# Performance work log

Measured on AMD Instinct MI355X. Metric: run time of the kernel, lower is better.

The kernel has to match this reference:

```python
import jax, jax.numpy as jnp
import numpy as np

H = 256    # hidden_size
NH = 8     # num_heads
B = 256    # batch_size (num graphs)
M = 128    # max_num_nodes per graph
N = B * M  # total nodes
E = N * 16 # total edges


def _bn(x, g, b, eps=1e-5):
    # BatchNorm1d in training mode: batch stats over node dim, biased variance
    m = x.mean(0)
    v = ((x - m) ** 2).mean(0)
    return g * (x - m) * jax.lax.rsqrt(v + eps) + b


def setup_inputs() -> dict:
    key = jax.random.key(0)
    ks = jax.random.split(key, 12)
    def lin(k, o, i):
        return jax.random.normal(k, (o, i), jnp.float32) / np.sqrt(i).astype(np.float32)
    return {
        "h": jax.random.normal(ks[0], (N, H), jnp.float32),
        "gin_w1": lin(ks[1], H, H), "gin_b1": jnp.zeros((H,), jnp.float32),
        "gin_w2": lin(ks[2], H, H), "gin_b2": jnp.zeros((H,), jnp.float32),
        "in_proj_w": lin(ks[3], 3 * H, H), "in_proj_b": jnp.zeros((3 * H,), jnp.float32),
        "out_proj_w": lin(ks[4], H, H), "out_proj_b": jnp.zeros((H,), jnp.float32),
        "bn_local_g": jnp.ones((H,), jnp.float32), "bn_local_b": jnp.zeros((H,), jnp.float32),
        "bn_attn_g": jnp.ones((H,), jnp.float32), "bn_attn_b": jnp.zeros((H,), jnp.float32),
        "bn_out_g": jnp.ones((H,), jnp.float32), "bn_out_b": jnp.zeros((H,), jnp.float32),
        "ffn1_w": lin(ks[5], 2 * H, H), "ffn1_b": jnp.zeros((2 * H,), jnp.float32),
        "ffn2_w": lin(ks[6], H, 2 * H), "ffn2_b": jnp.zeros((H,), jnp.float32),
        "edge_src": jax.random.randint(ks[7], (E,), 0, N, dtype=jnp.int32),
        "edge_dst": jax.random.randint(ks[8], (E,), 0, N, dtype=jnp.int32),
        "batch_num_nodes": jnp.full((B,), M, dtype=jnp.int32),
    }


def reference(h, gin_w1, gin_b1, gin_w2, gin_b2, in_proj_w, in_proj_b,
              out_proj_w, out_proj_b, bn_local_g, bn_local_b, bn_attn_g, bn_attn_b,
              bn_out_g, bn_out_b, ffn1_w, ffn1_b, ffn2_w, ffn2_b,
              edge_src, edge_dst, batch_num_nodes):
    # ---- local GIN conv: gin_nn((1+eps)*h + sum_neighbors h), eps=0 ----
    agg = jax.ops.segment_sum(h[edge_src], edge_dst, num_segments=N)
    z = h + agg
    z = jax.nn.relu(z @ gin_w1.T + gin_b1) @ gin_w2.T + gin_b2
    h_local = _bn(h + z, bn_local_g, bn_local_b)  # dropout=0

    # ---- to_dense_batch scatter indices ----
    cum = jnp.concatenate([jnp.zeros((1,), batch_num_nodes.dtype), jnp.cumsum(batch_num_nodes)])
    node = jnp.arange(N, dtype=jnp.int32)
    bid = jnp.searchsorted(cum[1:], node, side='right')  # graph id per node
    idx = node - cum[bid] + bid * M                      # slot in dense [B*M]
    hd = jnp.zeros((B * M, H), h.dtype).at[idx].set(h).reshape(B, M, H)
    mask = jnp.zeros((B * M,), bool).at[idx].set(True).reshape(B, M)

    # ---- MultiheadAttention (batch_first, self-attn, key_padding_mask) ----
    qkv = hd @ in_proj_w.T + in_proj_b
    q, k, v = jnp.split(qkv, 3, axis=-1)
    dh = H // NH
    q = q.reshape(B, M, NH, dh)
    k = k.reshape(B, M, NH, dh)
    v = v.reshape(B, M, NH, dh)
    scores = jnp.einsum('bqhd,bkhd->bhqk', q, k) / np.float32(np.sqrt(dh))
    scores = jnp.where(mask[:, None, None, :], scores, jnp.float32(-1e9))
    attn = jax.nn.softmax(scores, axis=-1)
    ao = jnp.einsum('bhqk,bkhd->bqhd', attn, v).reshape(B, M, H)
    ao = ao @ out_proj_w.T + out_proj_b
    h_attn = ao.reshape(B * M, H)[idx]  # ragged gather back (x[mask])
    h_attn = _bn(h + h_attn, bn_attn_g, bn_attn_b)

    # ---- combine + FFN + out norm ----
    hh = h_local + h_attn
    hh = hh + (jax.nn.relu(hh @ ffn1_w.T + ffn1_b) @ ffn2_w.T + ffn2_b)
    return _bn(hh, bn_out_g, bn_out_b)
```

## Files before the change

kernel.cpp:

```cpp
#include <hip/hip_runtime.h>

#define NNODES 32768
#define HDIM   256
#define NHEADS 8
#define NB     256
#define NEDGES 524288


typedef unsigned short u16;
typedef unsigned int   u32;
typedef unsigned long long u64;
typedef __attribute__((ext_vector_type(8))) short short8;
typedef __attribute__((ext_vector_type(4))) float f32x4;

__device__ __forceinline__ float bf2f(u16 u){
  union { u32 i; float f; } x; x.i = ((u32)u) << 16; return x.f;
}
__device__ __forceinline__ u16 f2bf(float f){
  union { float f; u32 i; } x; x.f = f;
  u32 r = x.i + 0x7fffu + ((x.i >> 16) & 1u);
  return (u16)(r >> 16);
}
__device__ __forceinline__ void unpack8(uint4 v, float* f){
  f[0] = bf2f((u16)(v.x & 0xffff)); f[1] = bf2f((u16)(v.x >> 16));
  f[2] = bf2f((u16)(v.y & 0xffff)); f[3] = bf2f((u16)(v.y >> 16));
  f[4] = bf2f((u16)(v.z & 0xffff)); f[5] = bf2f((u16)(v.z >> 16));
  f[6] = bf2f((u16)(v.w & 0xffff)); f[7] = bf2f((u16)(v.w >> 16));
}
__device__ __forceinline__ uint4 pack8(const float* f){
  uint4 v;
  v.x = (u32)f2bf(f[0]) | ((u32)f2bf(f[1]) << 16);
  v.y = (u32)f2bf(f[2]) | ((u32)f2bf(f[3]) << 16);
  v.z = (u32)f2bf(f[4]) | ((u32)f2bf(f[5]) << 16);
  v.w = (u32)f2bf(f[6]) | ((u32)f2bf(f[7]) << 16);
  return v;
}

typedef __attribute__((address_space(3))) unsigned int lds_u32;
typedef const __attribute__((address_space(1))) unsigned int gbl_u32;
__device__ __forceinline__ void gload16(const void* g, void* l){
  __builtin_amdgcn_global_load_lds((gbl_u32*)(u64)g,
                                   (lds_u32*)(u32)(u64)l, 16, 0, 0);
}

struct CvtPtrs { const void* p[19]; };

__device__ static const int CVT_CH[19] = {
  2097152,16384,64,16384,64,49152,192,16384,64,64,64,64,64,64,64,32768,128,32768,64};
__device__ static const int CVT_PR[19] = {
  0,8388608,8454144,8454400,8519936,8520192,8716800,8717568,8783104,
  8783360,8783616,8783872,8784128,8784384,8784640,8784896,8915968,8916480,9047552};
#define CVT_TOTAL_CHUNKS 2261952

__global__ __launch_bounds__(256) void convert_k(CvtPtrs cp, u16* __restrict__ dst,
    const int* __restrict__ edge_dst, int* __restrict__ counts){
  int gid = blockIdx.x * 256 + threadIdx.x;
  if (gid < NEDGES) atomicAdd(&counts[edge_dst[gid]], 1);
  if (gid >= CVT_TOTAL_CHUNKS) return;
  int t = 0, rem = gid;
  while (t < 18 && rem >= CVT_CH[t]) { rem -= CVT_CH[t]; t++; }
  u16* d = dst + CVT_PR[t] + (size_t)rem * 4;
  float4 v = ((const float4*)cp.p[t])[rem];
  u16 o[4] = { f2bf(v.x), f2bf(v.y), f2bf(v.z), f2bf(v.w) };
  *(uint2*)d = *(const uint2*)o;
}

__global__ void scan_k(const int* __restrict__ counts, int* __restrict__ offsets,
                       int* __restrict__ cursor){
  __shared__ int part[1024];
  int t = threadIdx.x;
  int local[32];
  int s = 0;
  int base = t * 32;
#pragma unroll
  for (int i = 0; i < 32; i++){ local[i] = counts[base + i]; s += local[i]; }
  part[t] = s;
  __syncthreads();
  for (int off = 1; off < 1024; off <<= 1){
    int v = (t >= off) ? part[t - off] : 0;
    __syncthreads();
    part[t] += v;
    __syncthreads();
  }
  int run = part[t] - s;
#pragma unroll
  for (int i = 0; i < 32; i++){
    offsets[base + i] = run; cursor[base + i] = run; run += local[i];
  }
  if (t == 1023) offsets[NNODES] = run;
}

__global__ void bucket_k(const int* __restrict__ src, const int* __restrict__ dst,
                         int* __restrict__ cursor, int* __restrict__ srcs){
  int e = blockIdx.x * 256 + threadIdx.x;
  int p = atomicAdd(&cursor[dst[e]], 1);
  srcs[p] = src[e];
}

__global__ __launch_bounds__(256) void agg_k(const u16* __restrict__ h,
    const int* __restrict__ offsets, const int* __restrict__ srcs,
    u16* __restrict__ z0){
  int node = blockIdx.x * 4 + (threadIdx.x >> 6);
  int lane = threadIdx.x & 63;
  size_t coff = (size_t)lane * 4;
  int beg = offsets[node], end = offsets[node + 1];

  uint2 self = *(const uint2*)&h[(size_t)node * HDIM + coff];
  float a0 = bf2f((u16)(self.x & 0xffff)), a1 = bf2f((u16)(self.x >> 16));
  float a2 = bf2f((u16)(self.y & 0xffff)), a3 = bf2f((u16)(self.y >> 16));

  int e = beg;
  for (; e + 8 <= end; e += 8){
    uint2 v[8];
#pragma unroll
    for (int i = 0; i < 8; i++){
      int s = srcs[e + i];
      v[i] = *(const uint2*)&h[(size_t)s * HDIM + coff];
    }
#pragma unroll
    for (int i = 0; i < 8; i++){
      a0 += bf2f((u16)(v[i].x & 0xffff));
      a1 += bf2f((u16)(v[i].x >> 16));
      a2 += bf2f((u16)(v[i].y & 0xffff));
      a3 += bf2f((u16)(v[i].y >> 16));
    }
  }
  for (; e < end; e++){
    int s = srcs[e];
    uint2 va = *(const uint2*)&h[(size_t)s * HDIM + coff];
    a0 += bf2f((u16)(va.x & 0xffff));
    a1 += bf2f((u16)(va.x >> 16));
    a2 += bf2f((u16)(va.y & 0xffff));
    a3 += bf2f((u16)(va.y >> 16));
  }

  uint2 o;
  o.x = (u32)f2bf(a0) | ((u32)f2bf(a1) << 16);
  o.y = (u32)f2bf(a2) | ((u32)f2bf(a3) << 16);
  *(uint2*)&z0[(size_t)node * HDIM + coff] = o;
}

__device__ __forceinline__ void mfma_step(const u16* AS_, const u16* WS_,
    f32x4 (&acc)[4][4], int wm, int wn, int ln, int q4){
  short8 af[4], bfr[4];
#pragma unroll
  for (int mt = 0; mt < 4; mt++)
    af[mt] = *(const short8*)&AS_[(wm * 64 + mt * 16 + ln) * 32 + q4 * 8];
#pragma unroll
  for (int nt = 0; nt < 4; nt++)
    bfr[nt] = *(const short8*)&WS_[(wn * 64 + nt * 16 + ln) * 32 + q4 * 8];
#pragma unroll
  for (int mt = 0; mt < 4; mt++)
#pragma unroll
    for (int nt = 0; nt < 4; nt++)
      acc[mt][nt] = __builtin_amdgcn_mfma_f32_16x16x32_bf16(af[mt], bfr[nt], acc[mt][nt], 0, 0, 0);
}

template<int NO, int K, bool RELU, bool RES, bool STATS>
__global__ __launch_bounds__(256) void gemm_bt(const u16* __restrict__ A,
    const u16* __restrict__ W, const u16* __restrict__ bias,
    const u16* __restrict__ res, u16* __restrict__ C,
    float* __restrict__ ssum, float* __restrict__ ssq){
  __shared__ u16 As0[4096], Ws0[4096], As1[4096], Ws1[4096];
  const int tid = threadIdx.x;
  const int m0 = blockIdx.y * 128;
  const int n0 = blockIdx.x * 128;
  const int wave = tid >> 6, lane = tid & 63;
  const int wm = wave >> 1, wn = wave & 1;
  const int q4 = lane >> 4, ln = lane & 15;

  f32x4 acc[4][4] = {};

  const int r_l = tid >> 2;
  const int c_l = (tid & 3) * 8;
  const u16* gA = A + (size_t)(m0 + r_l) * K + c_l;
  const u16* gW = W + (size_t)(n0 + r_l) * K + c_l;
  u16* dA0 = As0 + wave * 512; u16* dW0 = Ws0 + wave * 512;
  u16* dA1 = As1 + wave * 512; u16* dW1 = Ws1 + wave * 512;

  const int NT = K / 32;

  gload16(gA, dA0); gload16(gA + 64 * K, dA0 + 2048);
  gload16(gW, dW0); gload16(gW + 64 * K, dW0 + 2048);
  __syncthreads();

#pragma unroll
  for (int t = 0; t < NT; t += 2){
    if (t + 1 < NT){
      int kn = (t + 1) * 32;
      gload16(gA + kn, dA1); gload16(gA + 64 * K + kn, dA1 + 2048);
      gload16(gW + kn, dW1); gload16(gW + 64 * K + kn, dW1 + 2048);
    }
    mfma_step(As0, Ws0, acc, wm, wn, ln, q4);
    __syncthreads();
    if (t + 2 < NT){
      int kn = (t + 2) * 32;
      gload16(gA + kn, dA0); gload16(gA + 64 * K + kn, dA0 + 2048);
      gload16(gW + kn, dW0); gload16(gW + 64 * K + kn, dW0 + 2048);
    }
    mfma_step(As1, Ws1, acc, wm, wn, ln, q4);
    __syncthreads();
  }

#pragma unroll
  for (int nt = 0; nt < 4; nt++){
    int col = n0 + wn * 64 + nt * 16 + ln;
    float bv = bf2f(bias[col]);
    float cs = 0.0f, cq = 0.0f;
#pragma unroll
    for (int mt = 0; mt < 4; mt++){
      int row = m0 + wm * 64 + mt * 16 + q4 * 4;
#pragma unroll
      for (int reg = 0; reg < 4; reg++){
        float v = acc[mt][nt][reg] + bv;
        if (RELU) v = fmaxf(v, 0.0f);
        if (RES)  v += bf2f(res[(size_t)(row + reg) * NO + col]);
        C[(size_t)(row + reg) * NO + col] = f2bf(v);
        if (STATS){ cs += v; cq += v * v; }
      }
    }
    if (STATS){
      cs += __shfl_xor(cs, 16); cs += __shfl_xor(cs, 32);
      cq += __shfl_xor(cq, 16); cq += __shfl_xor(cq, 32);
      if (lane < 16){
        atomicAdd(&ssum[col], cs);
        atomicAdd(&ssq[col], cq);
      }
    }
  }
}

__global__ __launch_bounds__(256) void attn_k(const u16* __restrict__ qkv,
                                              u16* __restrict__ ao){
  __shared__ u16 Qs[128 * 40];
  __shared__ u16 Ks[128 * 40];
  __shared__ u16 VTs[32 * 136];
  __shared__ u16 Ps[128 * 136];

  const int b  = blockIdx.x >> 3;
  const int nh = blockIdx.x & 7;
  const int tid = threadIdx.x;
  const int wave = tid >> 6, lane = tid & 63;
  const int q4 = lane >> 4, ln = lane & 15;

#pragma unroll
  for (int c2 = 0; c2 < 2; c2++){
    int chunk = tid + c2 * 256;
    int r = chunk >> 2;
    int cc = chunk & 3;
    size_t nb = (size_t)(b * 128 + r) * 768 + nh * 32 + cc * 8;
    uint4 vq = *(const uint4*)&qkv[nb];
    uint4 vk = *(const uint4*)&qkv[nb + 256];
    uint4 vv = *(const uint4*)&qkv[nb + 512];
    *(uint4*)&Qs[r * 40 + cc * 8] = vq;
    *(uint4*)&Ks[r * 40 + cc * 8] = vk;
    union { uint4 v; u16 h[8]; } uv; uv.v = vv;
#pragma unroll
    for (int i = 0; i < 8; i++) VTs[(cc * 8 + i) * 136 + r] = uv.h[i];
  }
  __syncthreads();

  f32x4 accs[2][8] = {};
  short8 qf[2];
#pragma unroll
  for (int mt = 0; mt < 2; mt++)
    qf[mt] = *(const short8*)&Qs[(wave * 32 + mt * 16 + ln) * 40 + q4 * 8];
#pragma unroll
  for (int nt = 0; nt < 8; nt++){
    short8 kf = *(const short8*)&Ks[(nt * 16 + ln) * 40 + q4 * 8];
    accs[0][nt] = __builtin_amdgcn_mfma_f32_16x16x32_bf16(qf[0], kf, accs[0][nt], 0, 0, 0);
    accs[1][nt] = __builtin_amdgcn_mfma_f32_16x16x32_bf16(qf[1], kf, accs[1][nt], 0, 0, 0);
  }

  const float scale = 0.17677669529663687f;
  float invs[2][4];
#pragma unroll
  for (int mt = 0; mt < 2; mt++){
#pragma unroll
    for (int reg = 0; reg < 4; reg++){
      float rm = -1e30f;
#pragma unroll
      for (int nt = 0; nt < 8; nt++){
        accs[mt][nt][reg] *= scale;
        rm = fmaxf(rm, accs[mt][nt][reg]);
      }
      for (int m = 1; m < 16; m <<= 1) rm = fmaxf(rm, __shfl_xor(rm, m));
      float rs = 0.0f;
#pragma unroll
      for (int nt = 0; nt < 8; nt++){
        float e = __expf(accs[mt][nt][reg] - rm);
        accs[mt][nt][reg] = e;
        rs += e;
      }
      for (int m = 1; m < 16; m <<= 1) rs += __shfl_xor(rs, m);
      invs[mt][reg] = 1.0f / rs;
    }
  }

#pragma unroll
  for (int mt = 0; mt < 2; mt++)
#pragma unroll
    for (int nt = 0; nt < 8; nt++)
#pragma unroll
      for (int reg = 0; reg < 4; reg++)
        Ps[(wave * 32 + mt * 16 + q4 * 4 + reg) * 136 + nt * 16 + ln] =
            f2bf(accs[mt][nt][reg] * invs[mt][reg]);
  __syncthreads();

  f32x4 acco[2][2] = {};
#pragma unroll
  for (int kk = 0; kk < 4; kk++){
    short8 pf[2], vf[2];
#pragma unroll
    for (int mt = 0; mt < 2; mt++)
      pf[mt] = *(const short8*)&Ps[(wave * 32 + mt * 16 + ln) * 136 + kk * 32 + q4 * 8];
#pragma unroll
    for (int nt = 0; nt < 2; nt++)
      vf[nt] = *(const short8*)&VTs[(nt * 16 + ln) * 136 + kk * 32 + q4 * 8];
#pragma unroll
    for (int mt = 0; mt < 2; mt++)
#pragma unroll
      for (int nt = 0; nt < 2; nt++)
        acco[mt][nt] = __builtin_amdgcn_mfma_f32_16x16x32_bf16(pf[mt], vf[nt], acco[mt][nt], 0, 0, 0);
  }

#pragma unroll
  for (int mt = 0; mt < 2; mt++)
#pragma unroll
    for (int nt = 0; nt < 2; nt++)
#pragma unroll
      for (int reg = 0; reg < 4; reg++){
        int node = b * 128 + wave * 32 + mt * 16 + q4 * 4 + reg;
        int col = nh * 32 + nt * 16 + ln;
        ao[(size_t)node * HDIM + col] = f2bf(acco[mt][nt][reg]);
      }
}

__global__ __launch_bounds__(256) void combine_k(const u16* __restrict__ xl,
    const u16* __restrict__ xa, const float* __restrict__ stats,
    const u16* __restrict__ gl, const u16* __restrict__ bl,
    const u16* __restrict__ ga, const u16* __restrict__ ba,
    u16* __restrict__ hh){
  __shared__ float cs0[256], cs1[256], cs2[256];
  int t = threadIdx.x;
  {
    const float invN = 1.0f / 32768.0f;
    float mA = stats[t] * invN;
    float vA = stats[256 + t] * invN - mA * mA;
    float sA = bf2f(gl[t]) * rsqrtf(vA + 1e-5f);
    float tA = bf2f(bl[t]) - mA * sA;
    float mB = stats[512 + t] * invN;
    float vB = stats[768 + t] * invN - mB * mB;
    float sB = bf2f(ga[t]) * rsqrtf(vB + 1e-5f);
    float tB = bf2f(ba[t]) - mB * sB;
    cs0[t] = sA; cs1[t] = sB; cs2[t] = tA + tB;
  }
  __syncthreads();
  int gid = blockIdx.x * 256 + t;
  size_t off = (size_t)gid * 8;
  int cb = (int)(off & 255);
  float sl[8], sa[8], tt[8];
  *(float4*)&sl[0] = *(const float4*)&cs0[cb];
  *(float4*)&sl[4] = *(const float4*)&cs0[cb + 4];
  *(float4*)&sa[0] = *(const float4*)&cs1[cb];
  *(float4*)&sa[4] = *(const float4*)&cs1[cb + 4];
  *(float4*)&tt[0] = *(const float4*)&cs2[cb];
  *(float4*)&tt[4] = *(const float4*)&cs2[cb + 4];
  float fl[8], fa[8], fo[8];
  unpack8(*(const uint4*)&xl[off], fl);
  unpack8(*(const uint4*)&xa[off], fa);
#pragma unroll
  for (int i = 0; i < 8; i++) fo[i] = sl[i] * fl[i] + sa[i] * fa[i] + tt[i];
  *(uint4*)&hh[off] = pack8(fo);
}

__global__ __launch_bounds__(256) void finalbn_k(const u16* __restrict__ y,
    const float* __restrict__ stats, const u16* __restrict__ g,
    const u16* __restrict__ bb, float* __restrict__ out){
  __shared__ float cs0[256], cs1[256];
  int t = threadIdx.x;
  {
    const float invN = 1.0f / 32768.0f;
    float m = stats[1024 + t] * invN;
    float v = stats[1280 + t] * invN - m * m;
    float s = bf2f(g[t]) * rsqrtf(v + 1e-5f);
    cs0[t] = s; cs1[t] = bf2f(bb[t]) - m * s;
  }
  __syncthreads();
  int gid = blockIdx.x * 256 + t;
  size_t off = (size_t)gid * 8;
  int cb = (int)(off & 255);
  float ss[8], tt[8];
  *(float4*)&ss[0] = *(const float4*)&cs0[cb];
  *(float4*)&ss[4] = *(const float4*)&cs0[cb + 4];
  *(float4*)&tt[0] = *(const float4*)&cs1[cb];
  *(float4*)&tt[4] = *(const float4*)&cs1[cb + 4];
  float fy[8], fo[8];
  unpack8(*(const uint4*)&y[off], fy);
#pragma unroll
  for (int i = 0; i < 8; i++) fo[i] = ss[i] * fy[i] + tt[i];
  *(float4*)&out[off] = *(const float4*)&fo[0];
  *(float4*)&out[off + 4] = *(const float4*)&fo[4];
}

extern "C" void kernel_launch(void* const* d_in, const int* in_sizes, int n_in,
                              void* d_out, int out_size, void* d_ws, size_t ws_size,
                              hipStream_t stream){
  const int* edge_src = (const int*)d_in[19];
  const int* edge_dst = (const int*)d_in[20];

  char* ws = (char*)d_ws;
  float* stats = (float*)ws;
  u16*   conv  = (u16*)(ws + 12288);
  u16*   A     = (u16*)(ws + 12288 + 18095616);
  u16*   B     = (u16*)(ws + 12288 + 18095616 + 16777216);
  u16*   C     = (u16*)d_out;
  const size_t BIG_NEED = 51662336ull + 50331648ull;
  const bool big = (ws_size >= BIG_NEED);
  u16* QKV = (u16*)(ws + 51662336);

  int* counts  = (int*)B;
  int* offsets = (int*)((char*)B + 131072);
  int* cursor  = (int*)((char*)B + 262400);
  int* srcs    = (int*)((char*)B + 393472);

  const u16* convH = conv;
  const u16* W1  = conv + 8388608; const u16* b1g = conv + 8454144;
  const u16* W2  = conv + 8454400; const u16* b2g = conv + 8519936;
  const u16* Win = conv + 8520192; const u16* bin = conv + 8716800;
  const u16* Wo  = conv + 8717568; const u16* bo  = conv + 8783104;
  const u16* g_l = conv + 8783360; const u16* b_l = conv + 8783616;
  const u16* g_a = conv + 8783872; const u16* b_a = conv + 8784128;
  const u16* g_o = conv + 8784384; const u16* b_o = conv + 8784640;
  const u16* Wf1 = conv + 8784896; const u16* bf1 = conv + 8915968;
  const u16* Wf2 = conv + 8916480; const u16* bf2 = conv + 9047552;

  hipMemsetAsync(ws, 0, 6144, stream);
  hipMemsetAsync(counts, 0, 131072, stream);

  CvtPtrs cp;
  for (int i = 0; i < 19; i++) cp.p[i] = d_in[i];
  convert_k<<<8836, 256, 0, stream>>>(cp, conv, edge_dst, counts);

  scan_k<<<1, 1024, 0, stream>>>(counts, offsets, cursor);
  bucket_k<<<NEDGES / 256, 256, 0, stream>>>(edge_src, edge_dst, cursor, srcs);
  agg_k<<<NNODES / 4, 256, 0, stream>>>(convH, offsets, srcs, A);

  gemm_bt<256, 256, true,  false, false><<<dim3(2, 256), 256, 0, stream>>>(
      A, W1, b1g, nullptr, B, nullptr, nullptr);
  gemm_bt<256, 256, false, true,  true ><<<dim3(2, 256), 256, 0, stream>>>(
      B, W2, b2g, convH, A, stats + 0, stats + 256);

  if (big){
    gemm_bt<768, 256, false, false, false><<<dim3(6, 256), 256, 0, stream>>>(
        convH, Win, bin, nullptr, QKV, nullptr, nullptr);
    attn_k<<<2048, 256, 0, stream>>>(QKV, C);
  } else {
    for (int c = 0; c < 4; c++){
      const u16* hA = convH + (size_t)c * 8192 * HDIM;
      u16* aoC = C + (size_t)c * 8192 * HDIM;
      gemm_bt<768, 256, false, false, false><<<dim3(6, 64), 256, 0, stream>>>(
          hA, Win, bin, nullptr, B, nullptr, nullptr);
      attn_k<<<512, 256, 0, stream>>>(B, aoC);
    }
  }

  gemm_bt<256, 256, false, true, true><<<dim3(2, 256), 256, 0, stream>>>(
      C, Wo, bo, convH, B, stats + 512, stats + 768);

  combine_k<<<4096, 256, 0, stream>>>(A, B, stats, g_l, b_l, g_a, b_a, C);

  gemm_bt<512, 256, true,  false, false><<<dim3(4, 256), 256, 0, stream>>>(
      C, Wf1, bf1, nullptr, A, nullptr, nullptr);
  gemm_bt<256, 512, false, true,  true ><<<dim3(2, 256), 256, 0, stream>>>(
      A, Wf2, bf2, C, (u16*)conv, stats + 1024, stats + 1280);

  finalbn_k<<<4096, 256, 0, stream>>>(conv, stats, g_o, b_o, (float*)d_out);
}
```

Baseline: 424.6 us.

## Stage GEMM and attention epilogues through LDS, fuse GIN1 with QKV GEMM

GEMM epilogues now write results into swizzled shared memory and then emit coalesced 16-byte global stores, with residual tiles also loaded into LDS in coalesced form. The attention output goes through LDS the same way. In the big-workspace path, the first GIN GEMM and the QKV projection share one launch (gemm_dual), and the stats memset is folded into scan_k. The aim is to replace scattered 2-byte stores and loads with coalesced vector traffic and to cut launches, at the cost of extra LDS traffic and barriers. The relu flag becomes a runtime value instead of a template parameter.

```diff
diff --git a/kernel.cpp b/kernel.cpp
--- a/kernel.cpp
+++ b/kernel.cpp
@@ -66,9 +66,11 @@
 }
 
 __global__ void scan_k(const int* __restrict__ counts, int* __restrict__ offsets,
-                       int* __restrict__ cursor){
+                       int* __restrict__ cursor, float* __restrict__ stats){
   __shared__ int part[1024];
   int t = threadIdx.x;
+  stats[t] = 0.0f;
+  if (t < 512) stats[1024 + t] = 0.0f;
   int local[32];
   int s = 0;
   int base = t * 32;
@@ -156,28 +158,21 @@
       acc[mt][nt] = __builtin_amdgcn_mfma_f32_16x16x32_bf16(af[mt], bfr[nt], acc[mt][nt], 0, 0, 0);
 }
 
-template<int NO, int K, bool RELU, bool RES, bool STATS>
-__global__ __launch_bounds__(256) void gemm_bt(const u16* __restrict__ A,
-    const u16* __restrict__ W, const u16* __restrict__ bias,
-    const u16* __restrict__ res, u16* __restrict__ C,
-    float* __restrict__ ssum, float* __restrict__ ssq){
-  __shared__ u16 As0[4096], Ws0[4096], As1[4096], Ws1[4096];
-  const int tid = threadIdx.x;
-  const int m0 = blockIdx.y * 128;
-  const int n0 = blockIdx.x * 128;
+template<int K>
+__device__ __forceinline__ void kloop(const u16* __restrict__ A,
+    const u16* __restrict__ W, u16* smem, int m0, int n0, int tid,
+    f32x4 (&acc)[4][4]){
+  u16* As0 = smem;        u16* Ws0 = smem + 4096;
+  u16* As1 = smem + 8192; u16* Ws1 = smem + 12288;
   const int wave = tid >> 6, lane = tid & 63;
   const int wm = wave >> 1, wn = wave & 1;
   const int q4 = lane >> 4, ln = lane & 15;
-
-  f32x4 acc[4][4] = {};
-
   const int r_l = tid >> 2;
   const int c_l = (tid & 3) * 8;
   const u16* gA = A + (size_t)(m0 + r_l) * K + c_l;
   const u16* gW = W + (size_t)(n0 + r_l) * K + c_l;
   u16* dA0 = As0 + wave * 512; u16* dW0 = Ws0 + wave * 512;
   u16* dA1 = As1 + wave * 512; u16* dW1 = Ws1 + wave * 512;
-
   const int NT = K / 32;
 
   gload16(gA, dA0); gload16(gA + 64 * K, dA0 + 2048);
@@ -201,21 +196,51 @@
     mfma_step(As1, Ws1, acc, wm, wn, ln, q4);
     __syncthreads();
   }
+}
+
+struct GemmCfg {
+  const u16* A; const u16* W; const u16* bias; const u16* res;
+  u16* C; float* ssum; float* ssq;
+  int NO; int nx; int relu;
+};
+
+template<bool RES, bool STATS>
+__device__ __forceinline__ void epilogue(f32x4 (&acc)[4][4], u16* smem,
+    const GemmCfg& c, int m0, int n0, int tid){
+  const int NO = c.NO;
+  const int wave = tid >> 6, lane = tid & 63;
+  const int wm = wave >> 1, wn = wave & 1;
+  const int q4 = lane >> 4, ln = lane & 15;
+
+  if (RES){
+#pragma unroll
+    for (int i = 0; i < 8; i++){
+      int ch = tid + i * 256;
+      int r = ch >> 4, k = ch & 15;
+      uint4 vv = *(const uint4*)&c.res[(size_t)(m0 + r) * NO + n0 + (k << 3)];
+      *(uint4*)&smem[r * 128 + ((((k >> 1) ^ (r & 7)) << 4)) + ((k & 1) << 3)] = vv;
+    }
+    __syncthreads();
+  }
 
 #pragma unroll
   for (int nt = 0; nt < 4; nt++){
-    int col = n0 + wn * 64 + nt * 16 + ln;
-    float bv = bf2f(bias[col]);
+    int lcol = wn * 64 + nt * 16 + ln;
+    int gcol = n0 + lcol;
+    float bv = bf2f(c.bias[gcol]);
+    int chunk = lcol >> 4;
     float cs = 0.0f, cq = 0.0f;
 #pragma unroll
     for (int mt = 0; mt < 4; mt++){
-      int row = m0 + wm * 64 + mt * 16 + q4 * 4;
+      int lrow = wm * 64 + mt * 16 + q4 * 4;
 #pragma unroll
       for (int reg = 0; reg < 4; reg++){
+        int r = lrow + reg;
+        int sidx = r * 128 + ((chunk ^ (r & 7)) << 4) + ln;
         float v = acc[mt][nt][reg] + bv;
-        if (RELU) v = fmaxf(v, 0.0f);
-        if (RES)  v += bf2f(res[(size_t)(row + reg) * NO + col]);
-        C[(size_t)(row + reg) * NO + col] = f2bf(v);
+        if (c.relu) v = fmaxf(v, 0.0f);
+        if (RES) v += bf2f(smem[sidx]);
+        smem[sidx] = f2bf(v);
         if (STATS){ cs += v; cq += v * v; }
       }
     }
@@ -223,11 +248,44 @@
       cs += __shfl_xor(cs, 16); cs += __shfl_xor(cs, 32);
       cq += __shfl_xor(cq, 16); cq += __shfl_xor(cq, 32);
       if (lane < 16){
-        atomicAdd(&ssum[col], cs);
-        atomicAdd(&ssq[col], cq);
+        atomicAdd(&c.ssum[gcol], cs);
+        atomicAdd(&c.ssq[gcol], cq);
       }
     }
   }
+  __syncthreads();
+
+#pragma unroll
+  for (int i = 0; i < 8; i++){
+    int ch = tid + i * 256;
+    int r = ch >> 4, k = ch & 15;
+    uint4 vv = *(const uint4*)&smem[r * 128 + (((k >> 1) ^ (r & 7)) << 4) + ((k & 1) << 3)];
+    *(uint4*)&c.C[(size_t)(m0 + r) * NO + n0 + (k << 3)] = vv;
+  }
+}
+
+template<int K, bool RES, bool STATS>
+__global__ __launch_bounds__(256) void gemm_one(GemmCfg c){
+  __shared__ u16 smem[16384];
+  const int tid = threadIdx.x;
+  const int m0 = blockIdx.y * 128;
+  const int n0 = blockIdx.x * 128;
+  f32x4 acc[4][4] = {};
+  kloop<K>(c.A, c.W, smem, m0, n0, tid, acc);
+  epilogue<RES, STATS>(acc, smem, c, m0, n0, tid);
+}
+
+__global__ __launch_bounds__(256) void gemm_dual(GemmCfg c0, GemmCfg c1, int split){
+  __shared__ u16 smem[16384];
+  const int tid = threadIdx.x;
+  const int fid = blockIdx.x;
+  GemmCfg c = (fid < split) ? c0 : c1;
+  int f = (fid < split) ? fid : fid - split;
+  const int m0 = (f / c.nx) * 128;
+  const int n0 = (f % c.nx) * 128;
+  f32x4 acc[4][4] = {};
+  kloop<256>(c.A, c.W, smem, m0, n0, tid, acc);
+  epilogue<false, false>(acc, smem, c, m0, n0, tid);
 }
 
 __global__ __launch_bounds__(256) void attn_k(const u16* __restrict__ qkv,
@@ -324,16 +382,24 @@
         acco[mt][nt] = __builtin_amdgcn_mfma_f32_16x16x32_bf16(pf[mt], vf[nt], acco[mt][nt], 0, 0, 0);
   }
 
+  __syncthreads();
+  u16* Os = Ps;
 #pragma unroll
   for (int mt = 0; mt < 2; mt++)
 #pragma unroll
     for (int nt = 0; nt < 2; nt++)
 #pragma unroll
-      for (int reg = 0; reg < 4; reg++){
-        int node = b * 128 + wave * 32 + mt * 16 + q4 * 4 + reg;
-        int col = nh * 32 + nt * 16 + ln;
-        ao[(size_t)node * HDIM + col] = f2bf(acco[mt][nt][reg]);
-      }
+      for (int reg = 0; reg < 4; reg++)
+        Os[(wave * 32 + mt * 16 + q4 * 4 + reg) * 40 + nt * 16 + ln] =
+            f2bf(acco[mt][nt][reg]);
+  __syncthreads();
+#pragma unroll
+  for (int i = 0; i < 2; i++){
+    int ch = tid + i * 256;
+    int r = ch >> 2, k = ch & 3;
+    uint4 vv = *(const uint4*)&Os[r * 40 + k * 8];
+    *(uint4*)&ao[(size_t)(b * 128 + r) * HDIM + nh * 32 + k * 8] = vv;
+  }
 }
 
 __global__ __launch_bounds__(256) void combine_k(const u16* __restrict__ xl,
@@ -413,16 +479,16 @@
   float* stats = (float*)ws;
   u16*   conv  = (u16*)(ws + 12288);
   u16*   A     = (u16*)(ws + 12288 + 18095616);
-  u16*   B     = (u16*)(ws + 12288 + 18095616 + 16777216);
+  u16*   Bb    = (u16*)(ws + 12288 + 18095616 + 16777216);
   u16*   C     = (u16*)d_out;
   const size_t BIG_NEED = 51662336ull + 50331648ull;
   const bool big = (ws_size >= BIG_NEED);
   u16* QKV = (u16*)(ws + 51662336);
 
-  int* counts  = (int*)B;
-  int* offsets = (int*)((char*)B + 131072);
-  int* cursor  = (int*)((char*)B + 262400);
-  int* srcs    = (int*)((char*)B + 393472);
+  int* counts  = (int*)Bb;
+  int* offsets = (int*)((char*)Bb + 131072);
+  int* cursor  = (int*)((char*)Bb + 262400);
+  int* srcs    = (int*)((char*)Bb + 393472);
 
   const u16* convH = conv;
   const u16* W1  = conv + 8388608; const u16* b1g = conv + 8454144;
@@ -435,45 +501,48 @@
   const u16* Wf1 = conv + 8784896; const u16* bf1 = conv + 8915968;
   const u16* Wf2 = conv + 8916480; const u16* bf2 = conv + 9047552;
 
-  hipMemsetAsync(ws, 0, 6144, stream);
   hipMemsetAsync(counts, 0, 131072, stream);
 
   CvtPtrs cp;
   for (int i = 0; i < 19; i++) cp.p[i] = d_in[i];
   convert_k<<<8836, 256, 0, stream>>>(cp, conv, edge_dst, counts);
 
-  scan_k<<<1, 1024, 0, stream>>>(counts, offsets, cursor);
+  scan_k<<<1, 1024, 0, stream>>>(counts, offsets, cursor, stats);
   bucket_k<<<NEDGES / 256, 256, 0, stream>>>(edge_src, edge_dst, cursor, srcs);
   agg_k<<<NNODES / 4, 256, 0, stream>>>(convH, offsets, srcs, A);
 
-  gemm_bt<256, 256, true,  false, false><<<dim3(2, 256), 256, 0, stream>>>(
-      A, W1, b1g, nullptr, B, nullptr, nullptr);
-  gemm_bt<256, 256, false, true,  true ><<<dim3(2, 256), 256, 0, stream>>>(
-      B, W2, b2g, convH, A, stats + 0, stats + 256);
-
   if (big){
-    gemm_bt<768, 256, false, false, false><<<dim3(6, 256), 256, 0, stream>>>(
-        convH, Win, bin, nullptr, QKV, nullptr, nullptr);
+    GemmCfg cg1  = { A,     W1,  b1g, nullptr, Bb,  nullptr, nullptr, 256, 2, 1 };
+    GemmCfg cqkv = { convH, Win, bin, nullptr, QKV, nullptr, nullptr, 768, 6, 0 };
+    gemm_dual<<<512 + 1536, 256, 0, stream>>>(cg1, cqkv, 512);
+
     attn_k<<<2048, 256, 0, stream>>>(QKV, C);
+
+    GemmCfg cg2 = { Bb, W2, b2g, convH, A, stats + 0, stats + 256, 256, 2, 0 };
+    gemm_one<256, true, true><<<dim3(2, 256), 256, 0, stream>>>(cg2);
   } else {
+    GemmCfg cg1 = { A, W1, b1g, nullptr, Bb, nullptr, nullptr, 256, 2, 1 };
+    gemm_one<256, false, false><<<dim3(2, 256), 256, 0, stream>>>(cg1);
+    GemmCfg cg2 = { Bb, W2, b2g, convH, A, stats + 0, stats + 256, 256, 2, 0 };
+    gemm_one<256, true, true><<<dim3(2, 256), 256, 0, stream>>>(cg2);
     for (int c = 0; c < 4; c++){
       const u16* hA = convH + (size_t)c * 8192 * HDIM;
       u16* aoC = C + (size_t)c * 8192 * HDIM;
-      gemm_bt<768, 256, false, false, false><<<dim3(6, 64), 256, 0, stream>>>(
-          hA, Win, bin, nullptr, B, nullptr, nullptr);
-      attn_k<<<512, 256, 0, stream>>>(B, aoC);
-    }
-  }
-
-  gemm_bt<256, 256, false, true, true><<<dim3(2, 256), 256, 0, stream>>>(
-      C, Wo, bo, convH, B, stats + 512, stats + 768);
-
-  combine_k<<<4096, 256, 0, stream>>>(A, B, stats, g_l, b_l, g_a, b_a, C);
-
-  gemm_bt<512, 256, true,  false, false><<<dim3(4, 256), 256, 0, stream>>>(
-      C, Wf1, bf1, nullptr, A, nullptr, nullptr);
-  gemm_bt<256, 512, false, true,  true ><<<dim3(2, 256), 256, 0, stream>>>(
-      A, Wf2, bf2, C, (u16*)conv, stats + 1024, stats + 1280);
+      GemmCfg cq = { hA, Win, bin, nullptr, Bb, nullptr, nullptr, 768, 6, 0 };
+      gemm_one<256, false, false><<<dim3(6, 64), 256, 0, stream>>>(cq);
+      attn_k<<<512, 256, 0, stream>>>(Bb, aoC);
+    }
+  }
+
+  GemmCfg cop = { C, Wo, bo, convH, Bb, stats + 512, stats + 768, 256, 2, 0 };
+  gemm_one<256, true, true><<<dim3(2, 256), 256, 0, stream>>>(cop);
+
+  combine_k<<<4096, 256, 0, stream>>>(A, Bb, stats, g_l, b_l, g_a, b_a, C);
+
+  GemmCfg cf1 = { C, Wf1, bf1, nullptr, A, nullptr, nullptr, 512, 4, 1 };
+  gemm_one<256, false, false><<<dim3(4, 256), 256, 0, stream>>>(cf1);
+  GemmCfg cf2 = { A, Wf2, bf2, C, (u16*)conv, stats + 1024, stats + 1280, 256, 2, 0 };
+  gemm_one<512, true, true><<<dim3(2, 256), 256, 0, stream>>>(cf2);
 
   finalbn_k<<<4096, 256, 0, stream>>>(conv, stats, g_o, b_o, (float*)d_out);
 }
```

Measured after the change: 424.8 us. No clear change (+0.1%).
